# Kernel tuning notes

Hardware: AMD Instinct MI355X
Metric: run time of the kernel (lower is better)

Reference implementation:

```python
import jax, jax.numpy as jnp
import numpy as np

D_MODEL = 1024
NUM_HEAD = 16
D_K = D_MODEL // NUM_HEAD


def setup_inputs() -> dict:
    key = jax.random.key(0)
    ks = jax.random.split(key, 11)
    B, S = 2, 2048
    s = 1.0 / np.sqrt(D_MODEL)
    return {
        "q": jax.random.normal(ks[0], (B, S, D_MODEL), jnp.float32),
        "k": jax.random.normal(ks[1], (B, S, D_MODEL), jnp.float32),
        "v": jax.random.normal(ks[2], (B, S, D_MODEL), jnp.float32),
        "Wq": jax.random.normal(ks[3], (D_MODEL, D_MODEL), jnp.float32) * s,
        "bq": jnp.zeros((D_MODEL,), jnp.float32),
        "Wk": jax.random.normal(ks[4], (D_MODEL, D_MODEL), jnp.float32) * s,
        "bk": jnp.zeros((D_MODEL,), jnp.float32),
        "Wv": jax.random.normal(ks[5], (D_MODEL, D_MODEL), jnp.float32) * s,
        "bv": jnp.zeros((D_MODEL,), jnp.float32),
        "Wo": jax.random.normal(ks[6], (D_MODEL, D_MODEL), jnp.float32) * s,
        "bo": jnp.zeros((D_MODEL,), jnp.float32),
    }


def _split_head(x, B):
    # [B, S, d_model] -> [B, H, S, d_k]
    S = x.shape[1]
    return x.reshape(B, S, NUM_HEAD, D_K).transpose(0, 2, 1, 3)


def reference(q, k, v, Wq, bq, Wk, bk, Wv, bv, Wo, bo):
    B = q.shape[0]
    qh = _split_head(q @ Wq + bq, B)  # [B,H,Sq,dk]
    kh = _split_head(k @ Wk + bk, B)  # [B,H,Sk,dk]
    vh = _split_head(v @ Wv + bv, B)  # [B,H,Sk,dk]
    scores = jnp.einsum("bhqd,bhkd->bhqk", qh, kh) / jnp.sqrt(
        jnp.asarray(D_K, qh.dtype)
    )
    attn = jax.nn.softmax(scores, axis=-1)
    out = jnp.einsum("bhqk,bhkd->bhqd", attn, vh)  # [B,H,Sq,dk]
    out = out.transpose(0, 2, 1, 3).reshape(B, -1, D_MODEL)
    return jax.nn.relu(out @ Wo + bo)
```

## Files before the change

### kernel.cpp

```cpp
#include <hip/hip_runtime.h>
#include <math.h>

#define SEQ 2048
#define NHD 16

typedef float f32x4 __attribute__((ext_vector_type(4), may_alias));
typedef _Float16 h16x8 __attribute__((ext_vector_type(8), may_alias));
typedef _Float16 h16x4 __attribute__((ext_vector_type(4), may_alias));

__device__ __forceinline__ void gl_lds16(const void* g, void* l) {
  __builtin_amdgcn_global_load_lds(
      (const __attribute__((address_space(1))) unsigned int*)g,
      (__attribute__((address_space(3))) unsigned int*)l, 16, 0, 0);
}

struct PrepArgs {
  const float* W[4];
  _Float16* T[4];
  const float* X[3];
  _Float16* H[3];
};

__global__ __launch_bounds__(256) void prep_k(PrepArgs a) {
  __shared__ float tile[64][65];
  const int blk = blockIdx.x;
  const int t = threadIdx.x;
  if (blk < 1024) {
    const int widx = blk >> 8, tl = blk & 255;
    const int nb = (tl & 15) * 64, kb = (tl >> 4) * 64;
    const float* __restrict__ W = a.W[widx];
    _Float16* __restrict__ T = a.T[widx];
    const int c = t & 63, r0 = t >> 6;
#pragma unroll
    for (int i = 0; i < 16; ++i) {
      const int r = i * 4 + r0;
      tile[r][c] = W[(size_t)(kb + r) * 1024 + nb + c];
    }
    __syncthreads();
#pragma unroll
    for (int i = 0; i < 16; ++i) {
      const int n = i * 4 + r0;
      T[(size_t)(nb + n) * 1024 + kb + c] = (_Float16)tile[c][n];
    }
  } else {
    const int b2 = blk - 1024;
    const int z = b2 >> 11, bx = b2 & 2047;
    const float* __restrict__ X = a.X[z];
    _Float16* __restrict__ H = a.H[z];
    const size_t i = ((size_t)bx * 256 + t) * 8;
    const f32x4 f0 = *(const f32x4*)(X + i);
    const f32x4 f1 = *(const f32x4*)(X + i + 4);
    const float fs[8] = {f0.x, f0.y, f0.z, f0.w, f1.x, f1.y, f1.z, f1.w};
    h16x8 o;
#pragma unroll
    for (int j = 0; j < 8; ++j) o[j] = (_Float16)fs[j];
    *(h16x8*)(H + i) = o;
  }
}

__global__ __launch_bounds__(256) void vtrans_k(const unsigned short* __restrict__ Vb,
                                                unsigned short* __restrict__ Vt) {
  __shared__ unsigned short tile[64][65];
  const int t = threadIdx.x;
  const int c = t & 63, r0 = t >> 6;
  const int s0 = blockIdx.x * 64;
  const int bh = blockIdx.y;
#pragma unroll
  for (int i = 0; i < 16; ++i) {
    const int r = i * 4 + r0;
    tile[r][c] = Vb[((size_t)bh * SEQ + s0 + r) * 64 + c];
  }
  __syncthreads();
#pragma unroll
  for (int i = 0; i < 16; ++i) {
    const int d = i * 4 + r0;
    const int sp = ((c & 15) * 4) + (c >> 4);
    Vt[((size_t)bh * 64 + d) * SEQ + s0 + sp] = tile[c][d];
  }
}

struct QKVArgs {
  const _Float16* A[3];
  const _Float16* Bt[3];
  const float* bias[3];
  _Float16* C[3];
};

__global__ __launch_bounds__(512, 2) void gemm_qkv_k(QKVArgs a) {
  __shared__ __align__(16) char smem[131072];
  const int dblk = blockIdx.x;
  const int z = dblk >> 6;
  const int rb = dblk & 63;
  const int m0 = (rb >> 2) * 256;
  const int n0 = (rb & 3) * 256;
  const _Float16* __restrict__ A = a.A[z];
  const _Float16* __restrict__ Bt = a.Bt[z];
  const float* __restrict__ bias = a.bias[z];
  _Float16* __restrict__ C = a.C[z];

  const int t = threadIdx.x;
  const int l = t & 63, w = t >> 6;
  const int quad = l >> 4, l15 = l & 15;
  const int wm = w >> 2, wn = w & 3;

  const int srow = t >> 3;
  const int sslot = (t & 7) ^ (srow & 7);
  size_t goffA[4], goffB[4];
#pragma unroll
  for (int j = 0; j < 4; ++j) {
    goffA[j] = (size_t)(m0 + j * 64 + srow) * 1024 + sslot * 8;
    goffB[j] = (size_t)(n0 + j * 64 + srow) * 1024 + sslot * 8;
  }

  auto stage = [&](int buf, int kt) {
    const int k0 = kt * 64;
    char* base = smem + buf * 65536;
#pragma unroll
    for (int j = 0; j < 4; ++j) {
      gl_lds16(A + goffA[j] + k0, base + j * 8192 + w * 1024);
      gl_lds16(Bt + goffB[j] + k0, base + 32768 + j * 8192 + w * 1024);
    }
  };

  const f32x4 z4 = {0.f, 0.f, 0.f, 0.f};
  f32x4 acc[8][4];
#pragma unroll
  for (int i = 0; i < 8; ++i)
#pragma unroll
    for (int j = 0; j < 4; ++j) acc[i][j] = z4;

  const int xr = l15 & 7;

  stage(0, 0);
  for (int kt = 0; kt < 16; ++kt) {
    const int cur = kt & 1;
    if (kt < 15) {
      stage(cur ^ 1, kt + 1);
      asm volatile("s_waitcnt vmcnt(8)" ::: "memory");
    } else {
      asm volatile("s_waitcnt vmcnt(0)" ::: "memory");
    }
    __builtin_amdgcn_sched_barrier(0);
    __builtin_amdgcn_s_barrier();

    const char* base = smem + cur * 65536;
    h16x8 bf[4][2];
#pragma unroll
    for (int nj = 0; nj < 4; ++nj) {
      const int rowB = wn * 64 + nj * 16 + l15;
#pragma unroll
      for (int h = 0; h < 2; ++h) {
        const int sl = (h * 4 + quad) ^ xr;
        bf[nj][h] = *(const h16x8*)(base + 32768 + rowB * 128 + sl * 16);
      }
    }
#pragma unroll
    for (int mi = 0; mi < 8; ++mi) {
      const int rowA = wm * 128 + mi * 16 + l15;
      const h16x8 af0 = *(const h16x8*)(base + rowA * 128 + ((quad ^ xr) * 16));
      const h16x8 af1 = *(const h16x8*)(base + rowA * 128 + (((4 + quad) ^ xr) * 16));
#pragma unroll
      for (int nj = 0; nj < 4; ++nj) {
        acc[mi][nj] = __builtin_amdgcn_mfma_f32_16x16x32_f16(af0, bf[nj][0], acc[mi][nj], 0, 0, 0);
        acc[mi][nj] = __builtin_amdgcn_mfma_f32_16x16x32_f16(af1, bf[nj][1], acc[mi][nj], 0, 0, 0);
      }
    }
    __builtin_amdgcn_sched_barrier(0);
    __builtin_amdgcn_s_barrier();
  }

#pragma unroll
  for (int mi = 0; mi < 8; ++mi)
#pragma unroll
    for (int nj = 0; nj < 4; ++nj) {
      const int col = n0 + wn * 64 + nj * 16 + l15;
      const float bv = bias[col];
#pragma unroll
      for (int r = 0; r < 4; ++r) {
        const int row = m0 + wm * 128 + mi * 16 + quad * 4 + r;
        const int b = row >> 11, s = row & 2047;
        const int h = col >> 6, d = col & 63;
        C[((size_t)(b * NHD + h) * SEQ + s) * 64 + d] = (_Float16)(acc[mi][nj][r] + bv);
      }
    }
}

__global__ __launch_bounds__(256) void gemm_o_k(
    const _Float16* __restrict__ Op0, const _Float16* __restrict__ Op1,
    const float* __restrict__ Lp, const _Float16* __restrict__ Bt,
    const float* __restrict__ bias, float* __restrict__ Cf) {
  __shared__ char smem[40960];
  float* inv_lds = (float*)(smem + 32768);
  const int rb = blockIdx.x;
  const int n0 = ((rb >> 3) & 7) * 128;
  const int m0 = ((((rb >> 6) << 3) | (rb & 7))) * 128;
  const int t = threadIdx.x;
  const int l = t & 63, w = t >> 6;
  const int quad = l >> 4, l15 = l & 15;
  const int wm = w >> 1, wn = w & 1;
  const int arow0 = t >> 2, aq = t & 3;

#pragma unroll
  for (int e = t; e < 2048; e += 256) {
    const int rl = e >> 4, hh = e & 15;
    const int m = m0 + rl;
    const int b = m >> 11, s = m & 2047;
    const size_t li = (size_t)(b * NHD + hh) * 2048 + s;
    inv_lds[e] = 1.f / (Lp[li] + Lp[65536 + li]);
  }
  __syncthreads();

  auto stageB = [&](int buf, int k0) {
#pragma unroll
    for (int it = 0; it < 2; ++it) {
      const int c = it * 4 + w;
      const int rr = c * 16 + l15;
      gl_lds16(Bt + (size_t)(n0 + rr) * 1024 + k0 + quad * 8,
               smem + buf * 8192 + c * 1024);
    }
  };
  auto loadA = [&](int k0, h16x8 (&r0)[2], h16x8 (&r1)[2]) {
#pragma unroll
    for (int it = 0; it < 2; ++it) {
      const size_t off = (size_t)(m0 + it * 64 + arow0) * 1024 + k0 + aq * 8;
      r0[it] = *(const h16x8*)(Op0 + off);
      r1[it] = *(const h16x8*)(Op1 + off);
    }
  };
  auto writeA = [&](int buf, int k0, const h16x8 (&r0)[2], const h16x8 (&r1)[2]) {
    const int head = k0 >> 6;
    h16x8* alds = (h16x8*)(smem + 16384 + buf * 8192);
#pragma unroll
    for (int it = 0; it < 2; ++it) {
      const int row = it * 64 + arow0;
      const int slot = (row >> 4) * 64 + aq * 16 + ((row & 15) ^ (aq * 2));
      const float inv = inv_lds[row * 16 + head];
      h16x8 hv;
#pragma unroll
      for (int j = 0; j < 8; ++j)
        hv[j] = (_Float16)(((float)r0[it][j] + (float)r1[it][j]) * inv);
      alds[slot] = hv;
    }
  };

  const f32x4 z4 = {0.f, 0.f, 0.f, 0.f};
  f32x4 acc[4][4];
#pragma unroll
  for (int i = 0; i < 4; ++i)
#pragma unroll
    for (int j = 0; j < 4; ++j) acc[i][j] = z4;

  h16x8 a0r[2], a1r[2];
  loadA(0, a0r, a1r);
  stageB(0, 0);
  writeA(0, 0, a0r, a1r);
  __syncthreads();
  int cur = 0;
  for (int k0 = 0; k0 < 1024; k0 += 32) {
    const int nk = k0 + 32;
    if (nk < 1024) {
      loadA(nk, a0r, a1r);
      stageB(cur ^ 1, nk);
    }
    const h16x8* blds = (const h16x8*)(smem + cur * 8192);
    const h16x8* alds = (const h16x8*)(smem + 16384 + cur * 8192);
    h16x8 af[4], bf[4];
#pragma unroll
    for (int i = 0; i < 4; ++i) {
      af[i] = alds[(wm * 4 + i) * 64 + quad * 16 + (l15 ^ (quad * 2))];
      bf[i] = blds[(wn * 4 + i) * 64 + l];
    }
#pragma unroll
    for (int i = 0; i < 4; ++i)
#pragma unroll
      for (int j = 0; j < 4; ++j)
        acc[i][j] = __builtin_amdgcn_mfma_f32_16x16x32_f16(af[i], bf[j], acc[i][j], 0, 0, 0);
    if (nk < 1024) writeA(cur ^ 1, nk, a0r, a1r);
    __syncthreads();
    cur ^= 1;
  }
#pragma unroll
  for (int i = 0; i < 4; ++i)
#pragma unroll
    for (int j = 0; j < 4; ++j) {
      const int col = n0 + wn * 64 + j * 16 + l15;
      const float bv = bias[col];
#pragma unroll
      for (int r = 0; r < 4; ++r) {
        const int row = m0 + wm * 64 + i * 16 + quad * 4 + r;
        Cf[(size_t)row * 1024 + col] = fmaxf(acc[i][j][r] + bv, 0.f);
      }
    }
}

__global__ __launch_bounds__(256, 4) void attn_k(
    const _Float16* __restrict__ Qf, const _Float16* __restrict__ Kf,
    const _Float16* __restrict__ Vtp,
    _Float16* __restrict__ Op0, _Float16* __restrict__ Op1,
    float* __restrict__ Lp) {
  __shared__ char smem[34816];
  h16x8* lds8 = (h16x8*)smem;
  const int dblk = blockIdx.x;
  const int comb = ((dblk >> 7) << 3) | (dblk & 7);
  const int q0 = ((dblk >> 3) & 15) * 128;
  const int bh = comb >> 1;
  const int kz = comb & 1;
  const int t = threadIdx.x;
  const int l = t & 63, w = t >> 6;
  const int quad = l >> 4, l15 = l & 15;
  const int b = bh >> 4, h = bh & 15;

  const _Float16* Kb = Kf + (size_t)bh * SEQ * 64;
  const _Float16* Vtb = Vtp + (size_t)bh * 64 * SEQ;

  h16x8 qf[2][2];
#pragma unroll
  for (int mi = 0; mi < 2; ++mi) {
    const size_t qb = ((size_t)bh * SEQ + q0 + w * 32 + mi * 16 + l15) * 64;
#pragma unroll
    for (int ks = 0; ks < 2; ++ks)
      qf[mi][ks] = *(const h16x8*)&Qf[qb + ks * 32 + quad * 8];
  }
  const f32x4 z4 = {0.f, 0.f, 0.f, 0.f};
  f32x4 oacc[2][4], lacc[2];
#pragma unroll
  for (int mi = 0; mi < 2; ++mi) {
    lacc[mi] = z4;
#pragma unroll
    for (int i = 0; i < 4; ++i) oacc[mi][i] = z4;
  }
  h16x8 ones;
#pragma unroll
  for (int j = 0; j < 8; ++j) ones[j] = (_Float16)1.0f;

  const int kbeg = kz * 1024;
  for (int k0 = kbeg; k0 < kbeg + 1024; k0 += 64) {
#pragma unroll
    for (int it = 0; it < 2; ++it) {
      const int c = it * 4 + w;
      const int kd = (c >> 1) * 16 + l15;
      const int off2 = (c & 1) * 32 + quad * 8;
      gl_lds16(Kb + (size_t)(k0 + kd) * 64 + off2, smem + c * 1024);
      gl_lds16(Vtb + (size_t)kd * SEQ + k0 + off2, smem + 8192 + c * 1024);
    }
    __syncthreads();

    {
      h16x8 kfr[4][2];
#pragma unroll
      for (int nt = 0; nt < 4; ++nt)
#pragma unroll
        for (int ks = 0; ks < 2; ++ks) kfr[nt][ks] = lds8[(nt * 2 + ks) * 64 + l];

#pragma unroll
      for (int mi = 0; mi < 2; ++mi) {
        f32x4 sacc[4];
#pragma unroll
        for (int nt = 0; nt < 4; ++nt) {
          f32x4 s = z4;
          s = __builtin_amdgcn_mfma_f32_16x16x32_f16(qf[mi][0], kfr[nt][0], s, 0, 0, 0);
          s = __builtin_amdgcn_mfma_f32_16x16x32_f16(qf[mi][1], kfr[nt][1], s, 0, 0, 0);
          sacc[nt] = s;
        }
        char* pb = smem + 16384 + (w * 2 + mi) * 2304;
#pragma unroll
        for (int r = 0; r < 4; ++r) {
          h16x4 pk;
#pragma unroll
          for (int nt = 0; nt < 4; ++nt)
            pk[nt] = (_Float16)__expf(sacc[nt][r] * 0.125f);
          *(h16x4*)(pb + (quad * 4 + r) * 144 + l15 * 8) = pk;
        }
      }
    }
    __asm__ __volatile__("" ::: "memory");

    {
      h16x8 vfr[4][2];
#pragma unroll
      for (int nt = 0; nt < 4; ++nt)
#pragma unroll
        for (int ks = 0; ks < 2; ++ks) vfr[nt][ks] = lds8[512 + (nt * 2 + ks) * 64 + l];

#pragma unroll
      for (int mi = 0; mi < 2; ++mi) {
        char* pb = smem + 16384 + (w * 2 + mi) * 2304;
        const h16x8 pf0 = *(const h16x8*)(pb + l15 * 144 + quad * 16);
        const h16x8 pf1 = *(const h16x8*)(pb + l15 * 144 + 64 + quad * 16);
        lacc[mi] = __builtin_amdgcn_mfma_f32_16x16x32_f16(pf0, ones, lacc[mi], 0, 0, 0);
        lacc[mi] = __builtin_amdgcn_mfma_f32_16x16x32_f16(pf1, ones, lacc[mi], 0, 0, 0);
#pragma unroll
        for (int nt = 0; nt < 4; ++nt) {
          oacc[mi][nt] = __builtin_amdgcn_mfma_f32_16x16x32_f16(pf0, vfr[nt][0], oacc[mi][nt], 0, 0, 0);
          oacc[mi][nt] = __builtin_amdgcn_mfma_f32_16x16x32_f16(pf1, vfr[nt][1], oacc[mi][nt], 0, 0, 0);
        }
      }
    }
    __syncthreads();
  }

  _Float16* __restrict__ Op = kz ? Op1 : Op0;
#pragma unroll
  for (int mi = 0; mi < 2; ++mi)
#pragma unroll
    for (int nt = 0; nt < 4; ++nt)
#pragma unroll
      for (int r = 0; r < 4; ++r) {
        const size_t tok = (size_t)b * SEQ + q0 + w * 32 + mi * 16 + quad * 4 + r;
        Op[tok * 1024 + h * 64 + nt * 16 + l15] = (_Float16)oacc[mi][nt][r];
      }
  if (l15 == 0) {
#pragma unroll
    for (int mi = 0; mi < 2; ++mi)
#pragma unroll
      for (int r = 0; r < 4; ++r) {
        const int row = q0 + w * 32 + mi * 16 + quad * 4 + r;
        Lp[(size_t)kz * 65536 + bh * 2048 + row] = lacc[mi][r];
      }
  }
}

extern "C" void kernel_launch(void* const* d_in, const int* in_sizes, int n_in,
                              void* d_out, int out_size, void* d_ws, size_t ws_size,
                              hipStream_t stream) {
  const float* q = (const float*)d_in[0];
  const float* k = (const float*)d_in[1];
  const float* v = (const float*)d_in[2];
  const float* Wq = (const float*)d_in[3];
  const float* bq = (const float*)d_in[4];
  const float* Wk = (const float*)d_in[5];
  const float* bk = (const float*)d_in[6];
  const float* Wv = (const float*)d_in[7];
  const float* bv = (const float*)d_in[8];
  const float* Wo = (const float*)d_in[9];
  const float* bo = (const float*)d_in[10];

  char* W8 = (char*)d_ws;
  const size_t MB = 1024 * 1024;
  auto F = [&](size_t off) { return (_Float16*)(W8 + off); };
  _Float16* wt[4] = {F(0), F(2 * MB), F(4 * MB), F(6 * MB)};
  _Float16* qf = F(8 * MB);
  _Float16* kf = F(16 * MB);
  _Float16* vf = F(24 * MB);
  _Float16* Qf = F(32 * MB);
  _Float16* Kf = F(40 * MB);
  _Float16* Vb = F(48 * MB);
  _Float16* Vt = F(56 * MB);
  _Float16* Op0 = F(8 * MB);
  _Float16* Op1 = F(16 * MB);
  float* Lp = (float*)(W8 + 64 * MB);

  const dim3 blk(256);

  PrepArgs pa;
  pa.W[0] = Wq; pa.W[1] = Wk; pa.W[2] = Wv; pa.W[3] = Wo;
  pa.T[0] = wt[0]; pa.T[1] = wt[1]; pa.T[2] = wt[2]; pa.T[3] = wt[3];
  pa.X[0] = q; pa.X[1] = k; pa.X[2] = v;
  pa.H[0] = qf; pa.H[1] = kf; pa.H[2] = vf;
  prep_k<<<dim3(7168), blk, 0, stream>>>(pa);

  QKVArgs qa;
  qa.A[0] = qf; qa.A[1] = kf; qa.A[2] = vf;
  qa.Bt[0] = wt[0]; qa.Bt[1] = wt[1]; qa.Bt[2] = wt[2];
  qa.bias[0] = bq; qa.bias[1] = bk; qa.bias[2] = bv;
  qa.C[0] = Qf; qa.C[1] = Kf; qa.C[2] = Vb;
  gemm_qkv_k<<<dim3(192), dim3(512), 0, stream>>>(qa);

  vtrans_k<<<dim3(32, 32), blk, 0, stream>>>((const unsigned short*)Vb,
                                             (unsigned short*)Vt);
  attn_k<<<dim3(1024), blk, 0, stream>>>(Qf, Kf, Vt, Op0, Op1, Lp);
  gemm_o_k<<<dim3(256), blk, 0, stream>>>(Op0, Op1, Lp, wt[3], bo, (float*)d_out);
}
```

Measured before the change: 237.2 us.

## Double-buffer K tiles with split waitcnts, swizzle P layout, prescale Q

The attention loop now prefetches the next K tile into an alternate LDS buffer while the current one is consumed. V loads are issued early and waited on separately, using explicit vmcnt waits and raw s_barrier in place of __syncthreads. The P scratch buffer switches from a padded layout to an XOR-swizzled layout to avoid bank conflicts. Q is prescaled by 1/8 in fp16 once, removing a per-element multiply before exp. This raises LDS use to 40KB, which may reduce occupancy under launch_bounds(256,4), and the manual vmcnt counts must match the number of issued loads exactly.

```diff
diff --git a/kernel.cpp b/kernel.cpp
--- a/kernel.cpp
+++ b/kernel.cpp
@@ -298,8 +298,7 @@
     const _Float16* __restrict__ Vtp,
     _Float16* __restrict__ Op0, _Float16* __restrict__ Op1,
     float* __restrict__ Lp) {
-  __shared__ char smem[34816];
-  h16x8* lds8 = (h16x8*)smem;
+  __shared__ __align__(16) char smem[40960];
   const int dblk = blockIdx.x;
   const int comb = ((dblk >> 7) << 3) | (dblk & 7);
   const int q0 = ((dblk >> 3) & 15) * 128;
@@ -321,6 +320,12 @@
     for (int ks = 0; ks < 2; ++ks)
       qf[mi][ks] = *(const h16x8*)&Qf[qb + ks * 32 + quad * 8];
   }
+  const _Float16 qs = (_Float16)0.125f;
+#pragma unroll
+  for (int mi = 0; mi < 2; ++mi)
+#pragma unroll
+    for (int ks = 0; ks < 2; ++ks) qf[mi][ks] = qf[mi][ks] * qs;
+
   const f32x4 z4 = {0.f, 0.f, 0.f, 0.f};
   f32x4 oacc[2][4], lacc[2];
 #pragma unroll
@@ -333,24 +338,47 @@
 #pragma unroll
   for (int j = 0; j < 8; ++j) ones[j] = (_Float16)1.0f;
 
-  const int kbeg = kz * 1024;
-  for (int k0 = kbeg; k0 < kbeg + 1024; k0 += 64) {
+  auto stageK = [&](int buf, int k0) {
 #pragma unroll
     for (int it = 0; it < 2; ++it) {
       const int c = it * 4 + w;
       const int kd = (c >> 1) * 16 + l15;
       const int off2 = (c & 1) * 32 + quad * 8;
-      gl_lds16(Kb + (size_t)(k0 + kd) * 64 + off2, smem + c * 1024);
-      gl_lds16(Vtb + (size_t)kd * SEQ + k0 + off2, smem + 8192 + c * 1024);
-    }
-    __syncthreads();
+      gl_lds16(Kb + (size_t)(k0 + kd) * 64 + off2, smem + buf * 8192 + c * 1024);
+    }
+  };
+  auto stageV = [&](int k0) {
+#pragma unroll
+    for (int it = 0; it < 2; ++it) {
+      const int c = it * 4 + w;
+      const int kd = (c >> 1) * 16 + l15;
+      const int off2 = (c & 1) * 32 + quad * 8;
+      gl_lds16(Vtb + (size_t)kd * SEQ + k0 + off2, smem + 16384 + c * 1024);
+    }
+  };
+
+  const int kbeg = kz * 1024;
+  stageK(0, kbeg);
+  for (int kt = 0; kt < 16; ++kt) {
+    const int cur = kt & 1;
+    const int k0 = kbeg + kt * 64;
+    stageV(k0);
+    if (kt < 15) {
+      stageK(cur ^ 1, k0 + 64);
+      asm volatile("s_waitcnt vmcnt(4)" ::: "memory");
+    } else {
+      asm volatile("s_waitcnt vmcnt(2)" ::: "memory");
+    }
+    __builtin_amdgcn_sched_barrier(0);
+    __builtin_amdgcn_s_barrier();
 
     {
+      const h16x8* klds = (const h16x8*)(smem + cur * 8192);
       h16x8 kfr[4][2];
 #pragma unroll
       for (int nt = 0; nt < 4; ++nt)
 #pragma unroll
-        for (int ks = 0; ks < 2; ++ks) kfr[nt][ks] = lds8[(nt * 2 + ks) * 64 + l];
+        for (int ks = 0; ks < 2; ++ks) kfr[nt][ks] = klds[(nt * 2 + ks) * 64 + l];
 
 #pragma unroll
       for (int mi = 0; mi < 2; ++mi) {
@@ -362,31 +390,43 @@
           s = __builtin_amdgcn_mfma_f32_16x16x32_f16(qf[mi][1], kfr[nt][1], s, 0, 0, 0);
           sacc[nt] = s;
         }
-        char* pb = smem + 16384 + (w * 2 + mi) * 2304;
+        char* pb = smem + 24576 + (w * 2 + mi) * 2048;
 #pragma unroll
         for (int r = 0; r < 4; ++r) {
           h16x4 pk;
 #pragma unroll
           for (int nt = 0; nt < 4; ++nt)
-            pk[nt] = (_Float16)__expf(sacc[nt][r] * 0.125f);
-          *(h16x4*)(pb + (quad * 4 + r) * 144 + l15 * 8) = pk;
+            pk[nt] = (_Float16)__expf(sacc[nt][r]);
+          const int row = quad * 4 + r;
+          *(h16x4*)(pb + row * 128 + (((l15 >> 1) ^ (row & 7)) << 4) +
+                    ((l15 & 1) << 3)) = pk;
         }
       }
     }
     __asm__ __volatile__("" ::: "memory");
+    if (kt < 15) {
+      asm volatile("s_waitcnt vmcnt(2)" ::: "memory");
+    } else {
+      asm volatile("s_waitcnt vmcnt(0)" ::: "memory");
+    }
+    __builtin_amdgcn_sched_barrier(0);
+    __builtin_amdgcn_s_barrier();
 
     {
+      const h16x8* vlds = (const h16x8*)(smem + 16384);
       h16x8 vfr[4][2];
 #pragma unroll
       for (int nt = 0; nt < 4; ++nt)
 #pragma unroll
-        for (int ks = 0; ks < 2; ++ks) vfr[nt][ks] = lds8[512 + (nt * 2 + ks) * 64 + l];
+        for (int ks = 0; ks < 2; ++ks) vfr[nt][ks] = vlds[(nt * 2 + ks) * 64 + l];
 
 #pragma unroll
       for (int mi = 0; mi < 2; ++mi) {
-        char* pb = smem + 16384 + (w * 2 + mi) * 2304;
-        const h16x8 pf0 = *(const h16x8*)(pb + l15 * 144 + quad * 16);
-        const h16x8 pf1 = *(const h16x8*)(pb + l15 * 144 + 64 + quad * 16);
+        const char* pb = smem + 24576 + (w * 2 + mi) * 2048;
+        const h16x8 pf0 =
+            *(const h16x8*)(pb + l15 * 128 + ((quad ^ (l15 & 7)) << 4));
+        const h16x8 pf1 =
+            *(const h16x8*)(pb + l15 * 128 + (((4 + quad) ^ (l15 & 7)) << 4));
         lacc[mi] = __builtin_amdgcn_mfma_f32_16x16x32_f16(pf0, ones, lacc[mi], 0, 0, 0);
         lacc[mi] = __builtin_amdgcn_mfma_f32_16x16x32_f16(pf1, ones, lacc[mi], 0, 0, 0);
 #pragma unroll
@@ -396,7 +436,8 @@
         }
       }
     }
-    __syncthreads();
+    __asm__ __volatile__("" ::: "memory");
+    __builtin_amdgcn_s_barrier();
   }
 
   _Float16* __restrict__ Op = kz ? Op1 : Op0;
```

Result: slower. 248.5 us (+4.8%).

## Fuse V transpose into QKV GEMM epilogue and raise MFMA wave priority

Applied to the files above, without the earlier changes.

The QKV GEMM's V-projection blocks now stage their output tile in LDS and write it directly in the transposed, permuted Vt layout, which removes the separate vtrans kernel launch and its extra global round trip. The attention kernel also wraps its MFMA sections in s_setprio to favour waves issuing matrix ops. In exchange, the V blocks get a slower epilogue with an extra barrier and strided LDS reads.

```diff
diff --git a/kernel.cpp b/kernel.cpp
--- a/kernel.cpp
+++ b/kernel.cpp
@@ -55,27 +55,6 @@
 #pragma unroll
     for (int j = 0; j < 8; ++j) o[j] = (_Float16)fs[j];
     *(h16x8*)(H + i) = o;
-  }
-}
-
-__global__ __launch_bounds__(256) void vtrans_k(const unsigned short* __restrict__ Vb,
-                                                unsigned short* __restrict__ Vt) {
-  __shared__ unsigned short tile[64][65];
-  const int t = threadIdx.x;
-  const int c = t & 63, r0 = t >> 6;
-  const int s0 = blockIdx.x * 64;
-  const int bh = blockIdx.y;
-#pragma unroll
-  for (int i = 0; i < 16; ++i) {
-    const int r = i * 4 + r0;
-    tile[r][c] = Vb[((size_t)bh * SEQ + s0 + r) * 64 + c];
-  }
-  __syncthreads();
-#pragma unroll
-  for (int i = 0; i < 16; ++i) {
-    const int d = i * 4 + r0;
-    const int sp = ((c & 15) * 4) + (c >> 4);
-    Vt[((size_t)bh * 64 + d) * SEQ + s0 + sp] = tile[c][d];
   }
 }
 
@@ -169,20 +148,57 @@
     __builtin_amdgcn_s_barrier();
   }
 
-#pragma unroll
-  for (int mi = 0; mi < 8; ++mi)
-#pragma unroll
-    for (int nj = 0; nj < 4; ++nj) {
-      const int col = n0 + wn * 64 + nj * 16 + l15;
-      const float bv = bias[col];
-#pragma unroll
-      for (int r = 0; r < 4; ++r) {
-        const int row = m0 + wm * 128 + mi * 16 + quad * 4 + r;
-        const int b = row >> 11, s = row & 2047;
-        const int h = col >> 6, d = col & 63;
-        C[((size_t)(b * NHD + h) * SEQ + s) * 64 + d] = (_Float16)(acc[mi][nj][r] + bv);
-      }
-    }
+  if (z < 2) {
+#pragma unroll
+    for (int mi = 0; mi < 8; ++mi)
+#pragma unroll
+      for (int nj = 0; nj < 4; ++nj) {
+        const int col = n0 + wn * 64 + nj * 16 + l15;
+        const float bv = bias[col];
+#pragma unroll
+        for (int r = 0; r < 4; ++r) {
+          const int row = m0 + wm * 128 + mi * 16 + quad * 4 + r;
+          const int b = row >> 11, s = row & 2047;
+          const int h = col >> 6, d = col & 63;
+          C[((size_t)(b * NHD + h) * SEQ + s) * 64 + d] = (_Float16)(acc[mi][nj][r] + bv);
+        }
+      }
+  } else {
+    _Float16* sh = (_Float16*)smem;
+#pragma unroll
+    for (int mi = 0; mi < 8; ++mi)
+#pragma unroll
+      for (int nj = 0; nj < 4; ++nj) {
+        const int col = wn * 64 + nj * 16 + l15;
+        const float bv = bias[n0 + col];
+#pragma unroll
+        for (int r = 0; r < 4; ++r) {
+          const int row = wm * 128 + mi * 16 + quad * 4 + r;
+          sh[row * 256 + col] = (_Float16)(acc[mi][nj][r] + bv);
+        }
+      }
+    __syncthreads();
+    const int dr = t >> 1;
+    const int half = t & 1;
+    const int hh = dr >> 6, d = dr & 63;
+    const int b = m0 >> 11, sbase = m0 & 2047;
+    const int colL = hh * 64 + d;
+    const size_t gbase =
+        ((size_t)((b * NHD + (n0 >> 6) + hh) * 64 + d)) * SEQ + sbase + half * 128;
+#pragma unroll
+    for (int m8 = 0; m8 < 16; ++m8) {
+      const int qq = half * 128 + m8 * 8;
+      h16x8 ov;
+#pragma unroll
+      for (int j = 0; j < 8; ++j) {
+        const int q = qq + j;
+        const int g = q >> 6, p = q & 63;
+        const int c = (p >> 2) + ((p & 3) << 4);
+        ov[j] = sh[(g * 64 + c) * 256 + colL];
+      }
+      *(h16x8*)(C + gbase + m8 * 8) = ov;
+    }
+  }
 }
 
 __global__ __launch_bounds__(256) void gemm_o_k(
@@ -355,6 +371,7 @@
 #pragma unroll
       for (int mi = 0; mi < 2; ++mi) {
         f32x4 sacc[4];
+        __builtin_amdgcn_s_setprio(1);
 #pragma unroll
         for (int nt = 0; nt < 4; ++nt) {
           f32x4 s = z4;
@@ -362,6 +379,7 @@
           s = __builtin_amdgcn_mfma_f32_16x16x32_f16(qf[mi][1], kfr[nt][1], s, 0, 0, 0);
           sacc[nt] = s;
         }
+        __builtin_amdgcn_s_setprio(0);
         char* pb = smem + 16384 + (w * 2 + mi) * 2304;
 #pragma unroll
         for (int r = 0; r < 4; ++r) {
@@ -382,6 +400,7 @@
 #pragma unroll
         for (int ks = 0; ks < 2; ++ks) vfr[nt][ks] = lds8[512 + (nt * 2 + ks) * 64 + l];
 
+      __builtin_amdgcn_s_setprio(1);
 #pragma unroll
       for (int mi = 0; mi < 2; ++mi) {
         char* pb = smem + 16384 + (w * 2 + mi) * 2304;
@@ -395,6 +414,7 @@
           oacc[mi][nt] = __builtin_amdgcn_mfma_f32_16x16x32_f16(pf1, vfr[nt][1], oacc[mi][nt], 0, 0, 0);
         }
       }
+      __builtin_amdgcn_s_setprio(0);
     }
     __syncthreads();
   }
@@ -444,7 +464,6 @@
   _Float16* vf = F(24 * MB);
   _Float16* Qf = F(32 * MB);
   _Float16* Kf = F(40 * MB);
-  _Float16* Vb = F(48 * MB);
   _Float16* Vt = F(56 * MB);
   _Float16* Op0 = F(8 * MB);
   _Float16* Op1 = F(16 * MB);
@@ -463,11 +482,9 @@
   qa.A[0] = qf; qa.A[1] = kf; qa.A[2] = vf;
   qa.Bt[0] = wt[0]; qa.Bt[1] = wt[1]; qa.Bt[2] = wt[2];
   qa.bias[0] = bq; qa.bias[1] = bk; qa.bias[2] = bv;
-  qa.C[0] = Qf; qa.C[1] = Kf; qa.C[2] = Vb;
+  qa.C[0] = Qf; qa.C[1] = Kf; qa.C[2] = Vt;
   gemm_qkv_k<<<dim3(192), dim3(512), 0, stream>>>(qa);
 
-  vtrans_k<<<dim3(32, 32), blk, 0, stream>>>((const unsigned short*)Vb,
-                                             (unsigned short*)Vt);
   attn_k<<<dim3(1024), blk, 0, stream>>>(Qf, Kf, Vt, Op0, Op1, Lp);
   gemm_o_k<<<dim3(256), blk, 0, stream>>>(Op0, Op1, Lp, wt[3], bo, (float*)d_out);
 }
```

Measured after the change: 240.0 us. No clear change (+1.2%).
